# Kernel tuning notes

Hardware: AMD Instinct MI355X
Metric: run time of the kernel (lower is better)

The kernel has to match this reference:

```python
import jax, jax.numpy as jnp
import numpy as np

NUM_HEADS = 16
NUM_KV_HEADS = 4
ROPE_BASE = 10000.0
TRAIN_SEQ_LEN = 2048


def _rms_norm(x):
    eps = jnp.asarray(jnp.finfo(x.dtype).eps, x.dtype)
    return x * jax.lax.rsqrt(jnp.mean(x * x, axis=-1, keepdims=True) + eps)


def _rope_cos_sin(seq_len, head_dim, dtype):
    # seq_len <= TRAIN_SEQ_LEN -> no NTK rescaling, matches Rotary buffer path
    half = head_dim // 2
    inv_freq = 1.0 / (ROPE_BASE ** (jnp.arange(0, head_dim, 2, dtype=jnp.float32) / head_dim))
    t = jnp.arange(seq_len, dtype=jnp.float32)
    freqs = jnp.outer(t, inv_freq)  # [S, half]
    cos = jnp.cos(freqs)[None, :, None, :].astype(dtype)
    sin = jnp.sin(freqs)[None, :, None, :].astype(dtype)
    return cos, sin


def _apply_rotary(x, cos, sin):
    half = x.shape[-1] // 2
    x1, x2 = x[..., :half], x[..., half:]
    return jnp.concatenate([x1 * cos + x2 * sin, -x1 * sin + x2 * cos], axis=-1)


def setup_inputs() -> dict:
    key = jax.random.key(0)
    ks = jax.random.split(key, 5)
    B, S, D = 2, 2048, 2048
    kv_dim = NUM_KV_HEADS * (D // NUM_HEADS)
    sw = 0.02
    return {
        "x": jax.random.normal(ks[0], (B, S, D), jnp.float32),
        "Wq": jax.random.normal(ks[1], (D, D), jnp.float32) * sw,
        "Wk": jax.random.normal(ks[2], (kv_dim, D), jnp.float32) * sw,
        "Wv": jax.random.normal(ks[3], (kv_dim, D), jnp.float32) * sw,
        "Wproj": jax.random.normal(ks[4], (D, D), jnp.float32) * sw,
        "q_gain": jnp.ones((NUM_HEADS,), jnp.float32),
    }


def reference(x, Wq, Wk, Wv, Wproj, q_gain):
    B, S, D = x.shape
    H, Hkv = NUM_HEADS, NUM_KV_HEADS
    hd = D // H
    r = H // Hkv

    q = (x @ Wq.T).reshape(B, S, H, hd)
    k = (x @ Wk.T).reshape(B, S, Hkv, hd)
    v = (x @ Wv.T).reshape(B, S, Hkv, hd)

    q = _rms_norm(q)
    k = _rms_norm(k)

    cos, sin = _rope_cos_sin(S, hd, q.dtype)
    q = _apply_rotary(q, cos, sin)
    k = _apply_rotary(k, cos, sin)
    q = q * q_gain.astype(q.dtype)[None, None, :, None]

    # GQA: repeat kv heads (repeat_interleave along head dim)
    k = jnp.repeat(k, r, axis=2)  # [B,S,H,hd]
    v = jnp.repeat(v, r, axis=2)

    scale = 1.0 / jnp.sqrt(jnp.asarray(hd, q.dtype))
    scores = jnp.einsum("bqhd,bkhd->bhqk", q, k) * scale
    causal = jnp.tril(jnp.ones((S, S), dtype=bool))
    scores = jnp.where(causal[None, None], scores, jnp.asarray(-jnp.inf, scores.dtype))
    attn = jax.nn.softmax(scores, axis=-1)
    y = jnp.einsum("bhqk,bkhd->bqhd", attn, v)

    return y.reshape(B, S, D) @ Wproj.T
```

## Files before the change

### kernel.cpp

```cpp
#include <hip/hip_runtime.h>

#define D_MODEL 2048
#define SEQ 2048
#define BATCH 2
#define NH 16
#define NKV 4
#define HD 128
#define KVD (NKV * HD)
#define QKVN (D_MODEL + 2 * KVD)
#define MROWS (BATCH * SEQ)

typedef __attribute__((ext_vector_type(8))) short short8;
typedef __attribute__((ext_vector_type(4))) float f32x4;

__device__ __forceinline__ unsigned short f2bf(float f) {
    union { float f; unsigned int u; } v; v.f = f;
    unsigned int r = (v.u + 0x7FFFu + ((v.u >> 16) & 1u)) >> 16;
    return (unsigned short)r;
}

__device__ __forceinline__ unsigned short f2bf_pos(float f) {
    union { float f; unsigned int u; } v; v.f = f;
    return (unsigned short)((v.u + 0x8000u) >> 16);
}

__device__ __forceinline__ float bf2f(unsigned short u) {
    union { float f; unsigned int i; } v; v.i = ((unsigned int)u) << 16;
    return v.f;
}

__device__ __forceinline__ void async16(const void* g, void* l) {
    __builtin_amdgcn_global_load_lds((const __attribute__((address_space(1))) void*)g,
                                     (__attribute__((address_space(3))) void*)l, 16, 0, 0);
}

__global__ __launch_bounds__(256) void cast_all(const float* __restrict__ x,
                                                const float* __restrict__ wq,
                                                const float* __restrict__ wk,
                                                const float* __restrict__ wv,
                                                const float* __restrict__ wp,
                                                unsigned short* __restrict__ xb,
                                                unsigned short* __restrict__ wqkv,
                                                unsigned short* __restrict__ wpb) {
    int i = blockIdx.x * 256 + threadIdx.x;
    const float4* s; ushort4* d; int j;
    if (i < 2097152)      { s = (const float4*)x;  d = (ushort4*)xb;             j = i; }
    else if (i < 3145728) { s = (const float4*)wq; d = (ushort4*)wqkv;           j = i - 2097152; }
    else if (i < 3407872) { s = (const float4*)wk; d = (ushort4*)wqkv + 1048576; j = i - 3145728; }
    else if (i < 3670016) { s = (const float4*)wv; d = (ushort4*)wqkv + 1310720; j = i - 3407872; }
    else                  { s = (const float4*)wp; d = (ushort4*)wpb;            j = i - 3670016; }
    float4 v = s[j];
    ushort4 o;
    o.x = f2bf(v.x); o.y = f2bf(v.y); o.z = f2bf(v.z); o.w = f2bf(v.w);
    d[j] = o;
}

__global__ __launch_bounds__(256) void gemm_qkv(const unsigned short* __restrict__ A,
                                                const unsigned short* __restrict__ W,
                                                const float* __restrict__ gain,
                                                unsigned short* __restrict__ qbuf,
                                                unsigned short* __restrict__ kbuf,
                                                unsigned short* __restrict__ vtb) {
    __shared__ unsigned short smem[128 * 137];
    unsigned short* As = smem;
    unsigned short* Bs = smem + 4096;
    unsigned short* tile = smem;
    const int K = D_MODEL;
    const int tid  = threadIdx.x;
    const int lane = tid & 63;
    const int wave = tid >> 6;
    const int qm   = lane & 15;
    const int quad = lane >> 4;
    const int m0 = blockIdx.y * 128;
    const int bx = blockIdx.x;
    const int n0 = bx * 128;
    const int wm = (wave >> 1) * 64;
    const int wn = (wave & 1) * 64;

    f32x4 acc[4][4];
#pragma unroll
    for (int i = 0; i < 4; i++)
#pragma unroll
        for (int j = 0; j < 4; j++) acc[i][j] = (f32x4){0.f, 0.f, 0.f, 0.f};

    const int r1 = tid >> 2;
    const int c1 = (((tid & 3) ^ ((r1 >> 1) & 3)) * 8);
    const unsigned short* Ag = A + (size_t)(m0 + r1) * K + c1;
    const unsigned short* Wg = W + (size_t)(n0 + r1) * K + c1;
    unsigned short* AsW = &As[wave * 512];
    unsigned short* BsW = &Bs[wave * 512];
    const int swq = ((qm >> 1) & 3) * 8;

    for (int kt = 0; kt < K; kt += 32) {
        async16(Ag,                  AsW);
        async16(Ag + (size_t)64 * K, AsW + 2048);
        async16(Wg,                  BsW);
        async16(Wg + (size_t)64 * K, BsW + 2048);
        Ag += 32; Wg += 32;
        __syncthreads();
        short8 af[4], bfr[4];
#pragma unroll
        for (int mi = 0; mi < 4; mi++)
            af[mi] = *(const short8*)&As[(wm + mi * 16 + qm) * 32 + (quad * 8 ^ swq)];
#pragma unroll
        for (int ni = 0; ni < 4; ni++)
            bfr[ni] = *(const short8*)&Bs[(wn + ni * 16 + qm) * 32 + (quad * 8 ^ swq)];
#pragma unroll
        for (int mi = 0; mi < 4; mi++)
#pragma unroll
            for (int ni = 0; ni < 4; ni++)
                acc[mi][ni] = __builtin_amdgcn_mfma_f32_16x16x32_bf16(af[mi], bfr[ni], acc[mi][ni], 0, 0, 0);
        __syncthreads();
    }

#pragma unroll
    for (int mi = 0; mi < 4; mi++)
#pragma unroll
        for (int r = 0; r < 4; r++) {
            int row = wm + mi * 16 + quad * 4 + r;
#pragma unroll
            for (int ni = 0; ni < 4; ni++)
                tile[row * 137 + wn + ni * 16 + qm] = f2bf(acc[mi][ni][r]);
        }
    __syncthreads();

    const int s_base = m0 & 2047;
    const int bb = m0 >> 11;
    if (bx < 20) {
        const bool isq = bx < 16;
        const float g = isq ? gain[bx] * 0.12751744f : 1.0f;
        unsigned short* dst = isq
            ? qbuf + ((size_t)(bb * NH + bx) * SEQ + s_base) * HD
            : kbuf + ((size_t)(bb * NKV + (bx - 16)) * SEQ + s_base) * HD;
        const float inv_freq = __builtin_amdgcn_exp2f(-(float)lane * 0.20761871f);
        for (int rr = 0; rr < 32; rr++) {
            int row = wave * 32 + rr;
            float x1 = bf2f(tile[row * 137 + lane]);
            float x2 = bf2f(tile[row * 137 + 64 + lane]);
            float ss = x1 * x1 + x2 * x2;
            ss += __shfl_xor(ss, 1);  ss += __shfl_xor(ss, 2);  ss += __shfl_xor(ss, 4);
            ss += __shfl_xor(ss, 8);  ss += __shfl_xor(ss, 16); ss += __shfl_xor(ss, 32);
            float rs = rsqrtf(ss * (1.0f / 128.0f) + 1.1920929e-07f);
            float ang = (float)(s_base + row) * inv_freq;
            float sn, cs;
            sincosf(ang, &sn, &cs);
            float a1 = x1 * rs, a2 = x2 * rs;
            float o1 = (a1 * cs + a2 * sn) * g;
            float o2 = (a2 * cs - a1 * sn) * g;
            dst[(size_t)row * HD + lane]      = f2bf(o1);
            dst[(size_t)row * HD + 64 + lane] = f2bf(o2);
        }
    } else {
        const int hk = bx - 20;
        unsigned short* dst = vtb + ((size_t)(bb * NKV + hk) * HD) * SEQ + s_base;
        const int sc = (tid & 31) * 4;
        const int d0 = tid >> 5;
#pragma unroll
        for (int i = 0; i < 16; i++) {
            int d = d0 + 8 * i;
            ushort4 ov;
            ov.x = tile[(sc + 0) * 137 + d];
            ov.y = tile[(sc + 1) * 137 + d];
            ov.z = tile[(sc + 2) * 137 + d];
            ov.w = tile[(sc + 3) * 137 + d];
            *(ushort4*)(dst + (size_t)d * SEQ + sc) = ov;
        }
    }
}

__global__ __launch_bounds__(256) void gemm_bt(const unsigned short* __restrict__ A,
                                               const unsigned short* __restrict__ W,
                                               float* __restrict__ C, int M, int N, int K) {
    __shared__ unsigned short As[128 * 32];
    __shared__ unsigned short Bs[128 * 32];
    const int tid  = threadIdx.x;
    const int lane = tid & 63;
    const int wave = tid >> 6;
    const int qm   = lane & 15;
    const int quad = lane >> 4;
    const int m0 = blockIdx.y * 128;
    const int n0 = blockIdx.x * 128;
    const int wm = (wave >> 1) * 64;
    const int wn = (wave & 1) * 64;

    f32x4 acc[4][4];
#pragma unroll
    for (int i = 0; i < 4; i++)
#pragma unroll
        for (int j = 0; j < 4; j++) acc[i][j] = (f32x4){0.f, 0.f, 0.f, 0.f};

    const int r1 = tid >> 2;
    const int c1 = (((tid & 3) ^ ((r1 >> 1) & 3)) * 8);
    const unsigned short* Ag = A + (size_t)(m0 + r1) * K + c1;
    const unsigned short* Wg = W + (size_t)(n0 + r1) * K + c1;
    unsigned short* AsW = &As[wave * 512];
    unsigned short* BsW = &Bs[wave * 512];
    const int swq = ((qm >> 1) & 3) * 8;

    for (int kt = 0; kt < K; kt += 32) {
        async16(Ag,                  AsW);
        async16(Ag + (size_t)64 * K, AsW + 2048);
        async16(Wg,                  BsW);
        async16(Wg + (size_t)64 * K, BsW + 2048);
        Ag += 32; Wg += 32;
        __syncthreads();
        short8 af[4], bfr[4];
#pragma unroll
        for (int mi = 0; mi < 4; mi++)
            af[mi] = *(const short8*)&As[(wm + mi * 16 + qm) * 32 + (quad * 8 ^ swq)];
#pragma unroll
        for (int ni = 0; ni < 4; ni++)
            bfr[ni] = *(const short8*)&Bs[(wn + ni * 16 + qm) * 32 + (quad * 8 ^ swq)];
#pragma unroll
        for (int mi = 0; mi < 4; mi++)
#pragma unroll
            for (int ni = 0; ni < 4; ni++)
                acc[mi][ni] = __builtin_amdgcn_mfma_f32_16x16x32_bf16(af[mi], bfr[ni], acc[mi][ni], 0, 0, 0);
        __syncthreads();
    }
#pragma unroll
    for (int mi = 0; mi < 4; mi++) {
#pragma unroll
        for (int r = 0; r < 4; r++) {
            int row = m0 + wm + mi * 16 + quad * 4 + r;
            float* Crow = C + (size_t)row * N + n0 + wn + qm;
#pragma unroll
            for (int ni = 0; ni < 4; ni++) Crow[ni * 16] = acc[mi][ni][r];
        }
    }
}

__global__ __launch_bounds__(256, 4) void attn(const unsigned short* __restrict__ qb,
                                               const unsigned short* __restrict__ kb,
                                               const unsigned short* __restrict__ vt,
                                               const float* __restrict__ gain,
                                               unsigned short* __restrict__ y) {
    __shared__ unsigned short Ks[8192];
    __shared__ unsigned short Vs[8192];
    __shared__ unsigned short plds[4][1024];
    const int tid  = threadIdx.x;
    const int lane = tid & 63;
    const int wave = tid >> 6;
    const int bh   = blockIdx.x & 31;
    const int g4   = blockIdx.x >> 5;
    const int gg = g4 & 7;
    const int gs = g4 >> 3;
    const int qt64 = (gs == 0) ? gg : (gs == 1) ? (31 - gg) : (gs == 2) ? (8 + gg) : (23 - gg);
    const int h = bh & 15;
    const int b = bh >> 4;
    const int qm   = lane & 15;
    const int quad = lane >> 4;
    const int q0    = qt64 * 64;
    const int qrow0 = q0 + wave * 16;
    const float M = 17.0f * fabsf(gain[h]);

    const unsigned short* Qp = qb + (((size_t)(b * NH + h)) * SEQ + qrow0) * HD;
    const unsigned short* Kp = kb + ((size_t)(b * NKV + (h >> 2))) * SEQ * HD;
    const unsigned short* Vp = vt + ((size_t)(b * NKV + (h >> 2))) * HD * SEQ;

    short8 qf[4];
#pragma unroll
    for (int c = 0; c < 4; c++)
        qf[c] = *(const short8*)(Qp + qm * HD + c * 32 + quad * 8);

    f32x4 o[8];
#pragma unroll
    for (int t = 0; t < 8; t++) o[t] = (f32x4){0.f, 0.f, 0.f, 0.f};
    float lr[4] = {0.f, 0.f, 0.f, 0.f};

    const unsigned short* KsA = Kp + (size_t)(tid >> 4) * HD + (((tid & 15) ^ (tid >> 4)) & 15) * 8;
    const unsigned short* VsA = Vp + (size_t)(tid >> 3) * SEQ + (((tid & 7) ^ ((tid >> 3) & 7)) * 8);
    char* KsB = (char*)Ks + wave * 1024;
    char* VsB = (char*)Vs + wave * 1024;
    unsigned short* P = &plds[wave][0];

    const int kvend = q0 + 64;
    for (int kv0 = 0; kv0 < kvend; kv0 += 64) {
#pragma unroll
        for (int i = 0; i < 4; i++) {
            async16(KsA + (size_t)(16 * i) * HD,  KsB + i * 4096);
            async16(VsA + (size_t)(32 * i) * SEQ, VsB + i * 4096);
        }
        KsA += (size_t)64 * HD;
        VsA += 64;
        __syncthreads();

        f32x4 s[4];
#pragma unroll
        for (int g = 0; g < 4; g++) s[g] = (f32x4){0.f, 0.f, 0.f, 0.f};
#pragma unroll
        for (int c = 0; c < 4; c++) {
#pragma unroll
            for (int g = 0; g < 4; g++) {
                short8 kf = *(const short8*)&Ks[(g * 16 + qm) * 128 + (((c * 4 + quad) ^ qm) * 8)];
                s[g] = __builtin_amdgcn_mfma_f32_16x16x32_bf16(qf[c], kf, s[g], 0, 0, 0);
            }
        }
        if (kv0 + 63 > qrow0) {
#pragma unroll
            for (int g = 0; g < 4; g++)
#pragma unroll
                for (int r = 0; r < 4; r++) {
                    int qg = qrow0 + quad * 4 + r;
                    if (kv0 + g * 16 + qm > qg) s[g][r] = -3.0e38f;
                }
        }
        float p[4][4];
#pragma unroll
        for (int g = 0; g < 4; g++)
#pragma unroll
            for (int r = 0; r < 4; r++) {
                p[g][r] = __builtin_amdgcn_exp2f(s[g][r] - M);
                lr[r] += p[g][r];
            }
#pragma unroll
        for (int g = 0; g < 4; g++)
#pragma unroll
            for (int r = 0; r < 4; r++) {
                int rowp = quad * 4 + r;
                P[rowp * 64 + (((g * 2 + (qm >> 3)) ^ (rowp & 7)) * 8) + (qm & 7)] = f2bf_pos(p[g][r]);
            }
        short8 pa[2];
#pragma unroll
        for (int ka = 0; ka < 2; ka++)
            pa[ka] = *(const short8*)&P[qm * 64 + (((ka * 4 + quad) ^ (qm & 7)) * 8)];
#pragma unroll
        for (int t = 0; t < 8; t++) {
#pragma unroll
            for (int ka = 0; ka < 2; ka++) {
                short8 vf = *(const short8*)&Vs[(t * 16 + qm) * 64 + (((ka * 4 + quad) ^ (qm & 7)) * 8)];
                o[t] = __builtin_amdgcn_mfma_f32_16x16x32_bf16(pa[ka], vf, o[t], 0, 0, 0);
            }
        }
        __syncthreads();
    }
    float rl[4];
#pragma unroll
    for (int r = 0; r < 4; r++) {
        float l = lr[r];
        l += __shfl_xor(l, 1);
        l += __shfl_xor(l, 2);
        l += __shfl_xor(l, 4);
        l += __shfl_xor(l, 8);
        rl[r] = 1.0f / l;
    }
#pragma unroll
    for (int t = 0; t < 8; t++) {
#pragma unroll
        for (int r = 0; r < 4; r++) {
            size_t row = (size_t)(b * SEQ + qrow0 + quad * 4 + r);
            y[row * D_MODEL + h * HD + t * 16 + qm] = f2bf(o[t][r] * rl[r]);
        }
    }
}

extern "C" void kernel_launch(void* const* d_in, const int* in_sizes, int n_in,
                              void* d_out, int out_size, void* d_ws, size_t ws_size,
                              hipStream_t stream) {
    const float* x  = (const float*)d_in[0];
    const float* Wq = (const float*)d_in[1];
    const float* Wk = (const float*)d_in[2];
    const float* Wv = (const float*)d_in[3];
    const float* Wp = (const float*)d_in[4];
    const float* qg = (const float*)d_in[5];

    char* ws = (char*)d_ws;
    unsigned short* xb   = (unsigned short*)(ws + 0);
    unsigned short* wqkv = (unsigned short*)(ws + 16777216);
    unsigned short* wp   = (unsigned short*)(ws + 29360128);
    unsigned short* qbuf = (unsigned short*)(ws + 37748736);
    unsigned short* kbuf = (unsigned short*)(ws + 54525952);
    unsigned short* vtb  = (unsigned short*)(ws + 58720256);
    unsigned short* y    = xb;

    cast_all<<<18432, 256, 0, stream>>>(x, Wq, Wk, Wv, Wp, xb, wqkv, wp);
    gemm_qkv<<<dim3(24, 32), 256, 0, stream>>>(xb, wqkv, qg, qbuf, kbuf, vtb);
    attn<<<1024, 256, 0, stream>>>(qbuf, kbuf, vtb, qg, y);
    gemm_bt<<<dim3(16, 32), 256, 0, stream>>>(y, wp, (float*)d_out, MROWS, D_MODEL, D_MODEL);
}
```

Baseline: 296.6 us.

## Double-buffer GEMM K-loop with async prefetch and hardware sincos in RoPE

Both GEMM kernels (QKV projection and output projection) now use a double-buffered LDS pipeline over 64-wide K steps. Async loads for the next stage are issued before the MFMAs on the current stage, and partial vmcnt waits plus raw barriers replace the two full syncthreads per 32-wide step. MFMA blocks are wrapped in s_setprio. The RoPE epilogue swaps sincosf for range-reduced hardware sin/cos on revolutions, which is cheaper but slightly less accurate. The pipeline uses more LDS, which may cut occupancy, and the hand-written waitcnt/barrier sequencing adds ordering risk.

```diff
diff --git a/kernel.cpp b/kernel.cpp
--- a/kernel.cpp
+++ b/kernel.cpp
@@ -61,9 +61,9 @@
                                                 unsigned short* __restrict__ qbuf,
                                                 unsigned short* __restrict__ kbuf,
                                                 unsigned short* __restrict__ vtb) {
-    __shared__ unsigned short smem[128 * 137];
-    unsigned short* As = smem;
-    unsigned short* Bs = smem + 4096;
+    __shared__ unsigned short smem[32768];
+    unsigned short* Al = smem;
+    unsigned short* Bl = smem + 16384;
     unsigned short* tile = smem;
     const int K = D_MODEL;
     const int tid  = threadIdx.x;
@@ -84,34 +84,56 @@
         for (int j = 0; j < 4; j++) acc[i][j] = (f32x4){0.f, 0.f, 0.f, 0.f};
 
     const int r1 = tid >> 2;
-    const int c1 = (((tid & 3) ^ ((r1 >> 1) & 3)) * 8);
+    const int c1 = (((tid & 3) ^ ((tid >> 3) & 3)) * 8);
     const unsigned short* Ag = A + (size_t)(m0 + r1) * K + c1;
     const unsigned short* Wg = W + (size_t)(n0 + r1) * K + c1;
-    unsigned short* AsW = &As[wave * 512];
-    unsigned short* BsW = &Bs[wave * 512];
+    const int stg = wave * 512;
     const int swq = ((qm >> 1) & 3) * 8;
 
-    for (int kt = 0; kt < K; kt += 32) {
-        async16(Ag,                  AsW);
-        async16(Ag + (size_t)64 * K, AsW + 2048);
-        async16(Wg,                  BsW);
-        async16(Wg + (size_t)64 * K, BsW + 2048);
-        Ag += 32; Wg += 32;
-        __syncthreads();
-        short8 af[4], bfr[4];
-#pragma unroll
-        for (int mi = 0; mi < 4; mi++)
-            af[mi] = *(const short8*)&As[(wm + mi * 16 + qm) * 32 + (quad * 8 ^ swq)];
-#pragma unroll
-        for (int ni = 0; ni < 4; ni++)
-            bfr[ni] = *(const short8*)&Bs[(wn + ni * 16 + qm) * 32 + (quad * 8 ^ swq)];
-#pragma unroll
-        for (int mi = 0; mi < 4; mi++)
-#pragma unroll
-            for (int ni = 0; ni < 4; ni++)
-                acc[mi][ni] = __builtin_amdgcn_mfma_f32_16x16x32_bf16(af[mi], bfr[ni], acc[mi][ni], 0, 0, 0);
-        __syncthreads();
-    }
+#define STG_Q(khv, bufv) \
+    async16(Ag + (khv) * 32,                  &Al[(bufv) * 8192 + (khv) * 4096 + stg]); \
+    async16(Ag + (khv) * 32 + (size_t)64 * K, &Al[(bufv) * 8192 + (khv) * 4096 + 2048 + stg]); \
+    async16(Wg + (khv) * 32,                  &Bl[(bufv) * 8192 + (khv) * 4096 + stg]); \
+    async16(Wg + (khv) * 32 + (size_t)64 * K, &Bl[(bufv) * 8192 + (khv) * 4096 + 2048 + stg]);
+
+#define CMP_Q(bufv, khv) { \
+    short8 af[4], bfr[4]; \
+    _Pragma("unroll") \
+    for (int i = 0; i < 4; i++) { \
+        af[i]  = *(const short8*)&Al[(bufv) * 8192 + (khv) * 4096 + (wm + i * 16 + qm) * 32 + (quad * 8 ^ swq)]; \
+        bfr[i] = *(const short8*)&Bl[(bufv) * 8192 + (khv) * 4096 + (wn + i * 16 + qm) * 32 + (quad * 8 ^ swq)]; \
+    } \
+    __builtin_amdgcn_s_setprio(1); \
+    _Pragma("unroll") \
+    for (int mi = 0; mi < 4; mi++) \
+        _Pragma("unroll") \
+        for (int ni = 0; ni < 4; ni++) \
+            acc[mi][ni] = __builtin_amdgcn_mfma_f32_16x16x32_bf16(af[mi], bfr[ni], acc[mi][ni], 0, 0, 0); \
+    __builtin_amdgcn_s_setprio(0); \
+}
+
+    STG_Q(0, 0)
+    STG_Q(1, 0)
+    Ag += 64; Wg += 64;
+    asm volatile("s_waitcnt vmcnt(4)\n\ts_barrier" ::: "memory");
+
+    int buf = 0;
+    for (int t = 0; t < K / 64 - 1; ++t) {
+        STG_Q(0, buf ^ 1)
+        CMP_Q(buf, 0)
+        asm volatile("s_waitcnt vmcnt(4)\n\ts_barrier" ::: "memory");
+        STG_Q(1, buf ^ 1)
+        CMP_Q(buf, 1)
+        asm volatile("s_waitcnt vmcnt(4)\n\ts_barrier" ::: "memory");
+        Ag += 64; Wg += 64;
+        buf ^= 1;
+    }
+    CMP_Q(buf, 0)
+    asm volatile("s_waitcnt vmcnt(0)\n\ts_barrier" ::: "memory");
+    CMP_Q(buf, 1)
+    __syncthreads();
+#undef STG_Q
+#undef CMP_Q
 
 #pragma unroll
     for (int mi = 0; mi < 4; mi++)
@@ -132,7 +154,7 @@
         unsigned short* dst = isq
             ? qbuf + ((size_t)(bb * NH + bx) * SEQ + s_base) * HD
             : kbuf + ((size_t)(bb * NKV + (bx - 16)) * SEQ + s_base) * HD;
-        const float inv_freq = __builtin_amdgcn_exp2f(-(float)lane * 0.20761871f);
+        const float invf = __builtin_amdgcn_exp2f(-(float)lane * 0.20761871f - 2.6514961f);
         for (int rr = 0; rr < 32; rr++) {
             int row = wave * 32 + rr;
             float x1 = bf2f(tile[row * 137 + lane]);
@@ -141,9 +163,10 @@
             ss += __shfl_xor(ss, 1);  ss += __shfl_xor(ss, 2);  ss += __shfl_xor(ss, 4);
             ss += __shfl_xor(ss, 8);  ss += __shfl_xor(ss, 16); ss += __shfl_xor(ss, 32);
             float rs = rsqrtf(ss * (1.0f / 128.0f) + 1.1920929e-07f);
-            float ang = (float)(s_base + row) * inv_freq;
-            float sn, cs;
-            sincosf(ang, &sn, &cs);
+            float rev = (float)(s_base + row) * invf;
+            rev -= truncf(rev);
+            float sn = __builtin_amdgcn_sinf(rev);
+            float cs = __builtin_amdgcn_cosf(rev);
             float a1 = x1 * rs, a2 = x2 * rs;
             float o1 = (a1 * cs + a2 * sn) * g;
             float o2 = (a2 * cs - a1 * sn) * g;
@@ -171,8 +194,9 @@
 __global__ __launch_bounds__(256) void gemm_bt(const unsigned short* __restrict__ A,
                                                const unsigned short* __restrict__ W,
                                                float* __restrict__ C, int M, int N, int K) {
-    __shared__ unsigned short As[128 * 32];
-    __shared__ unsigned short Bs[128 * 32];
+    __shared__ unsigned short smem[32768];
+    unsigned short* Al = smem;
+    unsigned short* Bl = smem + 16384;
     const int tid  = threadIdx.x;
     const int lane = tid & 63;
     const int wave = tid >> 6;
@@ -190,34 +214,56 @@
         for (int j = 0; j < 4; j++) acc[i][j] = (f32x4){0.f, 0.f, 0.f, 0.f};
 
     const int r1 = tid >> 2;
-    const int c1 = (((tid & 3) ^ ((r1 >> 1) & 3)) * 8);
+    const int c1 = (((tid & 3) ^ ((tid >> 3) & 3)) * 8);
     const unsigned short* Ag = A + (size_t)(m0 + r1) * K + c1;
     const unsigned short* Wg = W + (size_t)(n0 + r1) * K + c1;
-    unsigned short* AsW = &As[wave * 512];
-    unsigned short* BsW = &Bs[wave * 512];
+    const int stg = wave * 512;
     const int swq = ((qm >> 1) & 3) * 8;
 
-    for (int kt = 0; kt < K; kt += 32) {
-        async16(Ag,                  AsW);
-        async16(Ag + (size_t)64 * K, AsW + 2048);
-        async16(Wg,                  BsW);
-        async16(Wg + (size_t)64 * K, BsW + 2048);
-        Ag += 32; Wg += 32;
-        __syncthreads();
-        short8 af[4], bfr[4];
-#pragma unroll
-        for (int mi = 0; mi < 4; mi++)
-            af[mi] = *(const short8*)&As[(wm + mi * 16 + qm) * 32 + (quad * 8 ^ swq)];
-#pragma unroll
-        for (int ni = 0; ni < 4; ni++)
-            bfr[ni] = *(const short8*)&Bs[(wn + ni * 16 + qm) * 32 + (quad * 8 ^ swq)];
-#pragma unroll
-        for (int mi = 0; mi < 4; mi++)
-#pragma unroll
-            for (int ni = 0; ni < 4; ni++)
-                acc[mi][ni] = __builtin_amdgcn_mfma_f32_16x16x32_bf16(af[mi], bfr[ni], acc[mi][ni], 0, 0, 0);
-        __syncthreads();
-    }
+#define STG_B(khv, bufv) \
+    async16(Ag + (khv) * 32,                  &Al[(bufv) * 8192 + (khv) * 4096 + stg]); \
+    async16(Ag + (khv) * 32 + (size_t)64 * K, &Al[(bufv) * 8192 + (khv) * 4096 + 2048 + stg]); \
+    async16(Wg + (khv) * 32,                  &Bl[(bufv) * 8192 + (khv) * 4096 + stg]); \
+    async16(Wg + (khv) * 32 + (size_t)64 * K, &Bl[(bufv) * 8192 + (khv) * 4096 + 2048 + stg]);
+
+#define CMP_B(bufv, khv) { \
+    short8 af[4], bfr[4]; \
+    _Pragma("unroll") \
+    for (int i = 0; i < 4; i++) { \
+        af[i]  = *(const short8*)&Al[(bufv) * 8192 + (khv) * 4096 + (wm + i * 16 + qm) * 32 + (quad * 8 ^ swq)]; \
+        bfr[i] = *(const short8*)&Bl[(bufv) * 8192 + (khv) * 4096 + (wn + i * 16 + qm) * 32 + (quad * 8 ^ swq)]; \
+    } \
+    __builtin_amdgcn_s_setprio(1); \
+    _Pragma("unroll") \
+    for (int mi = 0; mi < 4; mi++) \
+        _Pragma("unroll") \
+        for (int ni = 0; ni < 4; ni++) \
+            acc[mi][ni] = __builtin_amdgcn_mfma_f32_16x16x32_bf16(af[mi], bfr[ni], acc[mi][ni], 0, 0, 0); \
+    __builtin_amdgcn_s_setprio(0); \
+}
+
+    STG_B(0, 0)
+    STG_B(1, 0)
+    Ag += 64; Wg += 64;
+    asm volatile("s_waitcnt vmcnt(4)\n\ts_barrier" ::: "memory");
+
+    int buf = 0;
+    for (int t = 0; t < K / 64 - 1; ++t) {
+        STG_B(0, buf ^ 1)
+        CMP_B(buf, 0)
+        asm volatile("s_waitcnt vmcnt(4)\n\ts_barrier" ::: "memory");
+        STG_B(1, buf ^ 1)
+        CMP_B(buf, 1)
+        asm volatile("s_waitcnt vmcnt(4)\n\ts_barrier" ::: "memory");
+        Ag += 64; Wg += 64;
+        buf ^= 1;
+    }
+    CMP_B(buf, 0)
+    asm volatile("s_waitcnt vmcnt(0)\n\ts_barrier" ::: "memory");
+    CMP_B(buf, 1)
+#undef STG_B
+#undef CMP_B
+
 #pragma unroll
     for (int mi = 0; mi < 4; mi++) {
 #pragma unroll
```

Measured after the change: 297.7 us. About the same (+0.3%).
